# Kernel optimization log

Measured on AMD Instinct MI355X. Metric: run time of the kernel, lower is better.

Reference implementation:

```python
import jax, jax.numpy as jnp
import numpy as np

H, P, G, N, K, CS = 64, 64, 8, 128, 4, 256
HID = 2048
INTER = H * P                      # 4096
CONV_D = INTER + 2 * G * N         # 6144
PROJ = INTER + CONV_D + H          # 10304
EPS = 1e-5


def setup_inputs() -> dict:
    key = jax.random.key(0)
    ks = jax.random.split(key, 4)
    B_, L_ = 2, 2048
    return {
        "hidden_states": jax.random.normal(ks[0], (B_, L_, HID), jnp.float32),
        "in_proj_w": jax.random.normal(ks[1], (PROJ, HID), jnp.float32) * 0.02,
        "conv_w": jax.random.normal(ks[2], (CONV_D, K), jnp.float32) * 0.2,
        "conv_b": jnp.zeros((CONV_D,), jnp.float32),
        "dt_bias": jnp.ones((H,), jnp.float32),
        "A_log": jnp.log(jnp.arange(1, H + 1, dtype=jnp.float32)),
        "D": jnp.ones((H,), jnp.float32),
        "norm_w": jnp.ones((INTER,), jnp.float32),
        "out_proj_w": jax.random.normal(ks[3], (HID, INTER), jnp.float32) * 0.02,
    }


def reference(hidden_states, in_proj_w, conv_w, conv_b, dt_bias, A_log, D, norm_w, out_proj_w):
    b, l, _ = hidden_states.shape
    r = H // G  # heads per group

    zxbcdt = hidden_states @ in_proj_w.T                      # [b,l,PROJ]
    z = zxbcdt[..., :INTER]
    xBC = zxbcdt[..., INTER:INTER + CONV_D]
    dt = zxbcdt[..., INTER + CONV_D:]                          # [b,l,H]

    # causal depthwise conv1d (kernel K, left pad K-1) + SiLU
    xp = jnp.pad(xBC, ((0, 0), (K - 1, 0), (0, 0)))
    conv = conv_b
    for i in range(K):
        conv = conv + conv_w[:, i] * xp[:, i:i + l, :]
    xBC = jax.nn.silu(conv)

    x = xBC[..., :INTER]
    Bm = xBC[..., INTER:INTER + G * N]
    Cm = xBC[..., INTER + G * N:]

    dt = jax.nn.softplus(dt + dt_bias)                         # [b,l,H]
    A = -jnp.exp(A_log)                                        # [H]

    nc = l // CS
    x_c = x.reshape(b, nc, CS, G, r, P)
    dt_c = dt.reshape(b, nc, CS, G, r)
    B_c = Bm.reshape(b, nc, CS, G, N)
    C_c = Cm.reshape(b, nc, CS, G, N)

    dA = dt_c * A.reshape(G, r)                                # [b,nc,c,g,r]
    dA_cs = jnp.cumsum(dA, axis=2)                             # inclusive cumsum over chunk

    # intra-chunk: L[i,j] = exp(dA_cs[i]-dA_cs[j]) for i>=j
    diff = dA_cs[:, :, :, None] - dA_cs[:, :, None]            # [b,nc,i,j,g,r]
    mask = jnp.tril(jnp.ones((CS, CS), bool))[None, None, :, :, None, None]
    Lmat = jnp.exp(jnp.where(mask, diff, -jnp.inf))
    CB = jnp.einsum('bzign,bzjgn->bzijg', C_c, B_c)            # per-group C·B
    M = CB[..., None] * Lmat * dt_c[:, :, None]                # [b,nc,i,j,g,r]
    Y_diag = jnp.einsum('bzijgr,bzjgrp->bzigrp', M, x_c)

    # per-chunk end states
    w = jnp.exp(dA_cs[:, :, -1:] - dA_cs) * dt_c               # decay to chunk end * dt
    states = jnp.einsum('bzjgn,bzjgr,bzjgrp->bzgrpn', B_c, w, x_c)  # [b,nc,g,r,p,n]
    chunk_decay = jnp.exp(dA_cs[:, :, -1])                     # [b,nc,g,r]

    def step(S, inp):
        d, s = inp
        return d[..., None, None] * S + s, S                   # emit state BEFORE chunk

    init = jnp.zeros((b, G, r, P, N), x.dtype)
    _, prev = jax.lax.scan(step, init, (jnp.moveaxis(chunk_decay, 1, 0), jnp.moveaxis(states, 1, 0)))
    prev = jnp.moveaxis(prev, 0, 1)                            # [b,nc,g,r,p,n]

    Y_off = jnp.einsum('bzign,bzgrpn->bzigrp', C_c, prev) * jnp.exp(dA_cs)[..., None]

    Y = (Y_diag + Y_off).reshape(b, l, H, P) + D[:, None] * x.reshape(b, l, H, P)
    y = Y.reshape(b, l, INTER)

    # gated RMSNorm, norm_before_gate=True: out = rmsnorm(y) * silu(z)
    var = jnp.mean(y * y, axis=-1, keepdims=True)
    y = norm_w * (y * jax.lax.rsqrt(var + EPS)) * jax.nn.silu(z)

    return y @ out_proj_w.T
```

## Files before the change

kernel.cpp:

```cpp
#include <hip/hip_runtime.h>
#include <hip/hip_bf16.h>
#include <cstdint>
#include <cstddef>

#define H_     64
#define P_     64
#define G_     8
#define N_     128
#define K_     4
#define CS_    256
#define HID_   2048
#define INTER_ 4096
#define CONVD_ 6144
#define PROJ_  10304
#define ZSTR_  10240
#define B_     2
#define L_     2048
#define NC_    8
#define ML_    4096
#define EPS_   1e-5f

typedef unsigned short ushort_t;
typedef __attribute__((ext_vector_type(8))) short short8;
typedef __attribute__((ext_vector_type(4))) float f32x4;

__device__ inline float b2f(ushort_t v) {
  unsigned u = ((unsigned)v) << 16;
  float f;
  __builtin_memcpy(&f, &u, 4);
  return f;
}
__device__ inline ushort_t f2b(float f) {
  unsigned u;
  __builtin_memcpy(&u, &f, 4);
  u = u + 0x7FFFu + ((u >> 16) & 1u);
  return (ushort_t)(u >> 16);
}
__device__ inline void ld_bf8(const ushort_t* p, float* f) {
  uint4 u = *(const uint4*)p;
  const ushort_t* s = (const ushort_t*)&u;
#pragma unroll
  for (int c = 0; c < 8; ++c) f[c] = b2f(s[c]);
}
__device__ inline void st_bf8(ushort_t* p, const float* f) {
  uint4 u;
  ushort_t* s = (ushort_t*)&u;
#pragma unroll
  for (int c = 0; c < 8; ++c) s[c] = f2b(f[c]);
  *(uint4*)p = u;
}

__global__ __launch_bounds__(256) void cast1_k(const float* __restrict__ hs,
                                               const float* __restrict__ w_in,
                                               ushort_t* __restrict__ hsb,
                                               ushort_t* __restrict__ w_inb) {
  size_t e8 = ((size_t)blockIdx.x * 256 + threadIdx.x) * 8;
  const float* src;
  ushort_t* dst;
  const size_t HSN = (size_t)ML_ * HID_;
  if (e8 < HSN) { src = hs + e8; dst = hsb + e8; }
  else          { src = w_in + (e8 - HSN); dst = w_inb + (e8 - HSN); }
  float4 a = *(const float4*)src;
  float4 b = *(const float4*)(src + 4);
  float v[8] = {a.x, a.y, a.z, a.w, b.x, b.y, b.z, b.w};
  st_bf8(dst, v);
}

__global__ __launch_bounds__(256) void cast2_k(const float* __restrict__ w_out,
                                               ushort_t* __restrict__ w_outb) {
  size_t e8 = ((size_t)blockIdx.x * 256 + threadIdx.x) * 8;
  float4 a = *(const float4*)(w_out + e8);
  float4 b = *(const float4*)(w_out + e8 + 4);
  float v[8] = {a.x, a.y, a.z, a.w, b.x, b.y, b.z, b.w};
  st_bf8(w_outb + e8, v);
}

typedef const __attribute__((address_space(1))) unsigned int gu32;
typedef __attribute__((address_space(3))) unsigned int lu32;
__device__ __forceinline__ void gl_lds16(const ushort_t* g, ushort_t* l) {
  __builtin_amdgcn_global_load_lds((gu32*)g, (lu32*)l, 16, 0, 0);
}

template<int N> __device__ __forceinline__ void wait_vmcnt() {
  if constexpr (N == 8)      asm volatile("s_waitcnt vmcnt(8)" ::: "memory");
  else if constexpr (N == 6) asm volatile("s_waitcnt vmcnt(6)" ::: "memory");
  else if constexpr (N == 4) asm volatile("s_waitcnt vmcnt(4)" ::: "memory");
  else if constexpr (N == 3) asm volatile("s_waitcnt vmcnt(3)" ::: "memory");
  else                       asm volatile("s_waitcnt vmcnt(0)" ::: "memory");
}

template<int MR>
__device__ __forceinline__ void gemm_core(const ushort_t* __restrict__ Ag,
                                          const ushort_t* __restrict__ Bg,
                                          int lda, int ldb, int nkt,
                                          int bm, int bn, int brmax,
                                          ushort_t* __restrict__ As,
                                          ushort_t* __restrict__ Bs,
                                          f32x4 (&acc)[MR / 32][4]) {
  constexpr int MF = MR / 32;
  constexpr int ASLOT = MR * 32;
  constexpr int BSLOT = 256 * 32;
  constexpr int LPT = (MR == 256) ? 4 : 3;
  const int t = threadIdx.x;
  const int w = t >> 6, l = t & 63;
  const int wm = w >> 2, wn = w & 3;
  const int ml = l & 15, q = l >> 4;
  const int swz = (ml >> 1) & 3;
  const int aoff = (wm * (MR / 2) + ml) * 32 + ((q ^ swz) << 3);
  const int boff = (wn * 64 + ml) * 32 + ((q ^ swz) << 3);
  const int permc = (((l & 3) ^ ((l >> 3) & 3)) << 3);
  const ushort_t* ag0 = Ag + (size_t)(bm + (MR / 8) * w + (l >> 2)) * lda + permc;
  const ushort_t* ag1 = ag0 + (size_t)16 * lda;
  int br0 = bn + 32 * w + (l >> 2);      if (br0 > brmax) br0 = brmax;
  int br1 = bn + 32 * w + 16 + (l >> 2); if (br1 > brmax) br1 = brmax;
  const ushort_t* bg0 = Bg + (size_t)br0 * ldb + permc;
  const ushort_t* bg1 = Bg + (size_t)br1 * ldb + permc;
  ushort_t* alw = As + ((MR == 256) ? (2 * w * 512) : (w * 512));
  ushort_t* blw = Bs + 2 * w * 512;

#define STAGE_A_(kt_)                                                        \
  { const int k_ = (kt_) << 5;                                               \
    ushort_t* sa_ = alw + ((kt_) & 3) * ASLOT;                               \
    gl_lds16(ag0 + k_, sa_);                                                 \
    if (MR == 256) gl_lds16(ag1 + k_, sa_ + 512); }
#define STAGE_B_(kt_)                                                        \
  { const int k_ = (kt_) << 5;                                               \
    ushort_t* sb_ = blw + ((kt_) & 3) * BSLOT;                               \
    gl_lds16(bg0 + k_, sb_);                                                 \
    gl_lds16(bg1 + k_, sb_ + 512); }

  STAGE_A_(0); STAGE_B_(0);
  STAGE_A_(1); STAGE_B_(1);
  STAGE_A_(2); STAGE_B_(2);

#pragma unroll
  for (int i = 0; i < MF; ++i)
#pragma unroll
    for (int j = 0; j < 4; ++j) acc[i][j] = (f32x4){0.f, 0.f, 0.f, 0.f};

#pragma unroll 1
  for (int kt = 0; kt < nkt; ++kt) {
    const ushort_t* Asl = As + (kt & 3) * ASLOT;
    const ushort_t* Bsl = Bs + (kt & 3) * BSLOT;
    if (kt + 2 < nkt)      wait_vmcnt<2 * LPT>();
    else if (kt + 1 < nkt) wait_vmcnt<LPT>();
    else                   wait_vmcnt<0>();
    __builtin_amdgcn_s_barrier();
    asm volatile("" ::: "memory");
    const bool st = (kt + 3) < nkt;
    short8 bfr[4], af[MF / 2];
#pragma unroll
    for (int nf = 0; nf < 4; ++nf)
      bfr[nf] = *(const short8*)(Bsl + boff + nf * 512);
#pragma unroll
    for (int mf = 0; mf < MF / 2; ++mf)
      af[mf] = *(const short8*)(Asl + aoff + mf * 512);
    if (st) STAGE_A_(kt + 3);
    __builtin_amdgcn_s_setprio(1);
#pragma unroll
    for (int mf = 0; mf < MF / 2; ++mf)
#pragma unroll
      for (int nf = 0; nf < 4; ++nf)
        acc[mf][nf] = __builtin_amdgcn_mfma_f32_16x16x32_bf16(af[mf], bfr[nf], acc[mf][nf], 0, 0, 0);
    __builtin_amdgcn_s_setprio(0);
#pragma unroll
    for (int mf = 0; mf < MF / 2; ++mf)
      af[mf] = *(const short8*)(Asl + aoff + (mf + MF / 2) * 512);
    if (st) STAGE_B_(kt + 3);
    __builtin_amdgcn_s_setprio(1);
#pragma unroll
    for (int mf = 0; mf < MF / 2; ++mf)
#pragma unroll
      for (int nf = 0; nf < 4; ++nf)
        acc[mf + MF / 2][nf] = __builtin_amdgcn_mfma_f32_16x16x32_bf16(af[mf], bfr[nf], acc[mf + MF / 2][nf], 0, 0, 0);
    __builtin_amdgcn_s_setprio(0);
  }
#undef STAGE_A_
#undef STAGE_B_
}

__global__ __launch_bounds__(512, 2) void gemm1_256(const ushort_t* __restrict__ hsb,
                                                    const ushort_t* __restrict__ w_inb,
                                                    ushort_t* __restrict__ zb,
                                                    float* __restrict__ dtraw) {
  __shared__ __align__(16) ushort_t As[4 * 8192];
  __shared__ __align__(16) ushort_t Bs[4 * 8192];
  int bid = blockIdx.x;
  int wg = (bid & 7) * 82 + (bid >> 3);
  int tm = wg & 15, tn = wg >> 4;
  int bm = tm * 256, bn = tn * 256;
  f32x4 acc[8][4];
  gemm_core<256>(hsb, w_inb, HID_, HID_, HID_ / 32, bm, bn, PROJ_ - 1, As, Bs, acc);
  int t = threadIdx.x, w = t >> 6, l = t & 63;
  int wm = w >> 2, wn = w & 3, ml = l & 15, quad = l >> 4;
  int rb = bm + wm * 128 + quad * 4;
  int cb = bn + wn * 64 + ml;
  if (tn < 40) {
#pragma unroll
    for (int mf = 0; mf < 8; ++mf)
#pragma unroll
      for (int r = 0; r < 4; ++r) {
        size_t row = (size_t)(rb + mf * 16 + r) * ZSTR_;
#pragma unroll
        for (int nf = 0; nf < 4; ++nf)
          zb[row + cb + nf * 16] = f2b(acc[mf][nf][r]);
      }
  } else if (wn == 0) {
#pragma unroll
    for (int mf = 0; mf < 8; ++mf)
#pragma unroll
      for (int r = 0; r < 4; ++r) {
        size_t row = (size_t)(rb + mf * 16 + r) * 64;
#pragma unroll
        for (int nf = 0; nf < 4; ++nf)
          dtraw[row + ml + nf * 16] = acc[mf][nf][r];
      }
  }
}

__global__ __launch_bounds__(512, 2) void gemm2_128(const ushort_t* __restrict__ Ab,
                                                    const ushort_t* __restrict__ Bb,
                                                    float* __restrict__ C) {
  __shared__ __align__(16) ushort_t As[4 * 4096];
  __shared__ __align__(16) ushort_t Bs[4 * 8192];
  int bid = blockIdx.x;
  int wg = (bid & 7) * 32 + (bid >> 3);
  int tm = wg & 31, tn = wg >> 5;
  int bm = tm * 128, bn = tn * 256;
  f32x4 acc[4][4];
  gemm_core<128>(Ab, Bb, CONVD_, INTER_, INTER_ / 32, bm, bn, HID_ - 1, As, Bs, acc);
  int t = threadIdx.x, w = t >> 6, l = t & 63;
  int wm = w >> 2, wn = w & 3, ml = l & 15, quad = l >> 4;
  int rb = bm + wm * 64 + quad * 4;
  int cb = bn + wn * 64 + ml;
#pragma unroll
  for (int mf = 0; mf < 4; ++mf)
#pragma unroll
    for (int r = 0; r < 4; ++r) {
      size_t row = (size_t)(rb + mf * 16 + r) * HID_;
#pragma unroll
      for (int nf = 0; nf < 4; ++nf)
        C[row + cb + nf * 16] = acc[mf][nf][r];
    }
}

#define CROWS_ 8
__global__ __launch_bounds__(256) void conv_silu_k(const ushort_t* __restrict__ zb,
                                                   const float* __restrict__ cw,
                                                   const float* __restrict__ cb,
                                                   ushort_t* __restrict__ xcb) {
  int grp = blockIdx.x & 511;
  int seg = blockIdx.x >> 9;
  int u = threadIdx.x;
  int c8 = seg * 2048 + u * 8;
  int row0 = grp * CROWS_;
  int l0 = row0 & (L_ - 1);

  float wv[K_][8], bias[8];
  {
    const float4* wp = (const float4*)(cw + (size_t)c8 * K_);
#pragma unroll
    for (int c = 0; c < 8; ++c) {
      float4 w4 = wp[c];
      wv[0][c] = w4.x; wv[1][c] = w4.y; wv[2][c] = w4.z; wv[3][c] = w4.w;
    }
    float4 b0 = *(const float4*)(cb + c8);
    float4 b1 = *(const float4*)(cb + c8 + 4);
    bias[0] = b0.x; bias[1] = b0.y; bias[2] = b0.z; bias[3] = b0.w;
    bias[4] = b1.x; bias[5] = b1.y; bias[6] = b1.z; bias[7] = b1.w;
  }

  const ushort_t* xin = zb + (size_t)row0 * ZSTR_ + INTER_ + c8;
  ushort_t* xout = xcb + (size_t)row0 * CONVD_ + c8;

  float win[4][8];
#pragma unroll
  for (int i = 0; i < 3; ++i) {
    if (l0 > 0) {
      ld_bf8(xin + (ptrdiff_t)(i - 3) * ZSTR_, win[i]);
    } else {
#pragma unroll
      for (int c = 0; c < 8; ++c) win[i][c] = 0.f;
    }
  }
#pragma unroll
  for (int r = 0; r < CROWS_; ++r) {
    ld_bf8(xin + (size_t)r * ZSTR_, win[(r + 3) & 3]);
    float a[8];
#pragma unroll
    for (int c = 0; c < 8; ++c) {
      float v = bias[c];
      v = fmaf(wv[0][c], win[(r + 0) & 3][c], v);
      v = fmaf(wv[1][c], win[(r + 1) & 3][c], v);
      v = fmaf(wv[2][c], win[(r + 2) & 3][c], v);
      v = fmaf(wv[3][c], win[(r + 3) & 3][c], v);
      a[c] = v / (1.f + __expf(-v));
    }
    st_bf8(xout + (size_t)r * CONVD_, a);
  }
}

__global__ __launch_bounds__(256) void dt_scan_k(const float* __restrict__ dtraw,
                                                 const float* __restrict__ dt_bias,
                                                 const float* __restrict__ A_log,
                                                 float* __restrict__ dtp,
                                                 float* __restrict__ dacs,
                                                 float* __restrict__ cdec) {
  int bzh = blockIdx.x;
  int h = bzh & 63, z = (bzh >> 6) & 7, b = bzh >> 9;
  int i = threadIdx.x;
  size_t row = (size_t)b * L_ + z * CS_ + i;
  float dv = dtraw[row * 64 + h] + dt_bias[h];
  float sp = (dv > 20.f) ? dv : log1pf(expf(dv));
  float v = sp * (-expf(A_log[h]));
  __shared__ float sm[256];
  sm[i] = v;
  __syncthreads();
  for (int off = 1; off < 256; off <<= 1) {
    float add = (i >= off) ? sm[i - off] : 0.f;
    __syncthreads();
    sm[i] += add;
    __syncthreads();
  }
  float cs = sm[i];
  size_t ob = ((size_t)b * H_ + h) * L_ + z * CS_ + i;
  dtp[ob] = sp;
  dacs[ob] = cs;
  if (i == CS_ - 1) cdec[bzh] = expf(cs);
}

__global__ __launch_bounds__(256) void cb_k(const ushort_t* __restrict__ xcb,
                                            ushort_t* __restrict__ CBo) {
  int jt = blockIdx.x & 3, it = blockIdx.x >> 2;
  if (jt > it) return;
  int bzg = blockIdx.y;
  int g = bzg & 7, z = (bzg >> 3) & 7, b = bzg >> 6;
  int t = threadIdx.x;
  int tx = t & 15, ty = t >> 4;
  __shared__ float CtT[64][68];
  __shared__ float BtT[64][68];
  size_t rowbase = (size_t)b * L_ + (size_t)z * CS_;
  float acc[4][4];
#pragma unroll
  for (int i = 0; i < 4; ++i)
#pragma unroll
    for (int j = 0; j < 4; ++j) acc[i][j] = 0.f;

  for (int half = 0; half < 2; ++half) {
    int nb = half * 64;
    __syncthreads();
#pragma unroll
    for (int u = 0; u < 2; ++u) {
      int idx = t + u * 256;
      int rr = idx >> 3, f = idx & 7;
      float cv[8], bv[8];
      ld_bf8(xcb + (rowbase + it * 64 + rr) * CONVD_ + INTER_ + G_ * N_ + g * N_ + nb + f * 8, cv);
      ld_bf8(xcb + (rowbase + jt * 64 + rr) * CONVD_ + INTER_ + g * N_ + nb + f * 8, bv);
#pragma unroll
      for (int c = 0; c < 8; ++c) { CtT[f * 8 + c][rr] = cv[c]; BtT[f * 8 + c][rr] = bv[c]; }
    }
    __syncthreads();
    for (int n = 0; n < 64; ++n) {
      float4 cv = *(const float4*)&CtT[n][ty * 4];
      float4 bv = *(const float4*)&BtT[n][tx * 4];
      float cc[4] = {cv.x, cv.y, cv.z, cv.w};
      float bb[4] = {bv.x, bv.y, bv.z, bv.w};
#pragma unroll
      for (int i = 0; i < 4; ++i)
#pragma unroll
        for (int j = 0; j < 4; ++j) acc[i][j] = fmaf(cc[i], bb[j], acc[i][j]);
    }
  }
  size_t cbase = ((size_t)((b * 8 + z) * 8 + g)) * (CS_ * CS_);
#pragma unroll
  for (int i = 0; i < 4; ++i) {
    int row = it * 64 + ty * 4 + i;
    ushort4 v;
    v.x = f2b(acc[i][0]); v.y = f2b(acc[i][1]); v.z = f2b(acc[i][2]); v.w = f2b(acc[i][3]);
    *(ushort4*)(CBo + cbase + (size_t)row * CS_ + jt * 64 + tx * 4) = v;
  }
}

__global__ __launch_bounds__(256) void states_mfma(const ushort_t* __restrict__ xcb,
                                                   const float* __restrict__ dacs,
                                                   const float* __restrict__ dtp,
                                                   float* __restrict__ st) {
  int bzh = blockIdx.x;
  int h = bzh & 63, z = (bzh >> 6) & 7, b = bzh >> 9;
  int g = h >> 3;
  int t = threadIdx.x;
  int wv = t >> 6, lane = t & 63;
  int ml = lane & 15, ko = (lane >> 4) * 8;
  __shared__ float ws[256];
  __shared__ __align__(16) ushort_t Xw[64 * 136];
  __shared__ __align__(16) ushort_t Bt[128 * 136];
  size_t base = ((size_t)b * H_ + h) * L_ + z * CS_;
  float dlast = dacs[base + CS_ - 1];
  ws[t] = __expf(dlast - dacs[base + t]) * dtp[base + t];
  size_t rowbase = (size_t)b * L_ + z * CS_;
  f32x4 acc[4][2];
#pragma unroll
  for (int i = 0; i < 4; ++i) {
    acc[i][0] = (f32x4){0.f, 0.f, 0.f, 0.f};
    acc[i][1] = (f32x4){0.f, 0.f, 0.f, 0.f};
  }
  for (int half = 0; half < 2; ++half) {
    int j0 = half * 128;
    __syncthreads();
    {
      int jl = t >> 1, pseg = (t & 1) * 32;
      const ushort_t* xr = xcb + (rowbase + j0 + jl) * CONVD_ + h * P_ + pseg;
      float wj = ws[j0 + jl];
#pragma unroll
      for (int q = 0; q < 4; ++q) {
        float v[8];
        ld_bf8(xr + q * 8, v);
#pragma unroll
        for (int c = 0; c < 8; ++c) Xw[(pseg + q * 8 + c) * 136 + jl] = f2b(v[c] * wj);
      }
    }
    {
      int jl = t >> 1, nseg = (t & 1) * 64;
      const ushort_t* br = xcb + (rowbase + j0 + jl) * CONVD_ + INTER_ + g * N_ + nseg;
#pragma unroll
      for (int q = 0; q < 8; ++q) {
        uint4 raw = *(const uint4*)(br + q * 8);
        const ushort_t* s = (const ushort_t*)&raw;
#pragma unroll
        for (int c = 0; c < 8; ++c) Bt[(nseg + q * 8 + c) * 136 + jl] = s[c];
      }
    }
    __syncthreads();
#pragma unroll
    for (int k0 = 0; k0 < 128; k0 += 32) {
      short8 af[4], bf2[2];
#pragma unroll
      for (int mf = 0; mf < 4; ++mf)
        af[mf] = *(const short8*)(Xw + (mf * 16 + ml) * 136 + k0 + ko);
#pragma unroll
      for (int nf = 0; nf < 2; ++nf)
        bf2[nf] = *(const short8*)(Bt + (wv * 32 + nf * 16 + ml) * 136 + k0 + ko);
#pragma unroll
      for (int mf = 0; mf < 4; ++mf)
#pragma unroll
        for (int nf = 0; nf < 2; ++nf)
          acc[mf][nf] = __builtin_amdgcn_mfma_f32_16x16x32_bf16(af[mf], bf2[nf], acc[mf][nf], 0, 0, 0);
    }
  }
  float* outp = st + ((size_t)((b * 8 + z) * H_ + h)) * (P_ * N_);
  int quad = lane >> 4;
#pragma unroll
  for (int mf = 0; mf < 4; ++mf)
#pragma unroll
    for (int nf = 0; nf < 2; ++nf) {
      int n = wv * 32 + nf * 16 + ml;
#pragma unroll
      for (int r = 0; r < 4; ++r) {
        int p = mf * 16 + quad * 4 + r;
        outp[(size_t)p * N_ + n] = acc[mf][nf][r];
      }
    }
}

__global__ __launch_bounds__(256) void scan_k(float* __restrict__ st,
                                              const float* __restrict__ cdec) {
  size_t idx = (size_t)blockIdx.x * 256 + threadIdx.x;
  int b = (int)(idx >> 19);
  size_t rem = idx & 524287;
  int h = (int)(rem >> 13);
  float S = 0.f;
#pragma unroll
  for (int z = 0; z < NC_; ++z) {
    size_t off = (size_t)(b * 8 + z) * 524288 + rem;
    float old = st[off];
    st[off] = S;
    S = cdec[(b * 8 + z) * H_ + h] * S + old;
  }
}

__global__ __launch_bounds__(256) void y_mfma(const ushort_t* xcb,
                                              const ushort_t* __restrict__ CB,
                                              const float* __restrict__ pv,
                                              const float* __restrict__ dacs,
                                              const float* __restrict__ dtp,
                                              const float* __restrict__ Dw,
                                              ushort_t* Yx) {
  int bzh = blockIdx.x;
  int h = bzh & 63, z = (bzh >> 6) & 7, b = bzh >> 9;
  int g = h >> 3;
  int t = threadIdx.x;
  int wv = t >> 6, lane = t & 63;
  int ml = lane & 15, quad = lane >> 4, ko = quad * 8;
  __shared__ __align__(16) ushort_t Ms[256 * 40];
  __shared__ __align__(16) ushort_t XsYs[18432];
  __shared__ __align__(16) ushort_t Ps[64 * 136];
  __shared__ float dAs[256], dts[256];

  size_t rowbase = (size_t)b * L_ + z * CS_;
  {
    size_t base = ((size_t)b * H_ + h) * L_ + z * CS_;
    dAs[t] = dacs[base + t];
    dts[t] = dtp[base + t];
  }
  {
    int p = t >> 2, c0 = (t & 3) * 32;
    const float* pr = pv + ((size_t)((b * 8 + z) * H_ + h)) * (P_ * N_) + (size_t)p * N_ + c0;
    ushort_t* dst = Ps + p * 136 + c0;
#pragma unroll
    for (int u = 0; u < 4; ++u) {
      float4 a = *(const float4*)(pr + u * 8);
      float4 bq = *(const float4*)(pr + u * 8 + 4);
      float v[8] = {a.x, a.y, a.z, a.w, bq.x, bq.y, bq.z, bq.w};
      st_bf8(dst + u * 8, v);
    }
  }
  {
    const ushort_t* xr = xcb + (rowbase + t) * CONVD_ + h * P_;
    ushort_t* Xs = XsYs;
#pragma unroll
    for (int q = 0; q < 8; ++q) {
      uint4 raw = *(const uint4*)(xr + q * 8);
      const ushort_t* s = (const ushort_t*)&raw;
#pragma unroll
      for (int c = 0; c < 8; ++c) Xs[(q * 8 + c) * 264 + t] = s[c];
    }
  }

  f32x4 acc[4][4];
#pragma unroll
  for (int i = 0; i < 4; ++i)
#pragma unroll
    for (int j = 0; j < 4; ++j) acc[i][j] = (f32x4){0.f, 0.f, 0.f, 0.f};

  int cOff = INTER_ + G_ * N_ + g * N_;
#pragma unroll
  for (int k0 = 0; k0 < 128; k0 += 32) {
    __syncthreads();
#pragma unroll
    for (int u = 0; u < 4; ++u) {
      int sid = u * 256 + t;
      int row = sid >> 2, kc = (sid & 3) * 8;
      gl_lds16(xcb + (rowbase + row) * CONVD_ + cOff + k0 + kc,
               Ms + (size_t)(u * 256 + wv * 64) * 8);
    }
    __syncthreads();
    short8 af[4], bf[4];
#pragma unroll
    for (int mf = 0; mf < 4; ++mf)
      af[mf] = *(const short8*)(Ps + (mf * 16 + ml) * 136 + k0 + ko);
#pragma unroll
    for (int nf = 0; nf < 4; ++nf)
      bf[nf] = *(const short8*)(Ms + (wv * 64 + nf * 16 + ml) * 32 + ko);
#pragma unroll
    for (int mf = 0; mf < 4; ++mf)
#pragma unroll
      for (int nf = 0; nf < 4; ++nf)
        acc[mf][nf] = __builtin_amdgcn_mfma_f32_16x16x32_bf16(af[mf], bf[nf], acc[mf][nf], 0, 0, 0);
  }
#pragma unroll
  for (int nf = 0; nf < 4; ++nf) {
    float e = __expf(dAs[wv * 64 + nf * 16 + ml]);
#pragma unroll
    for (int mf = 0; mf < 4; ++mf) {
      acc[mf][nf][0] *= e; acc[mf][nf][1] *= e;
      acc[mf][nf][2] *= e; acc[mf][nf][3] *= e;
    }
  }

  float dAi_t = dAs[t];
  size_t cbase = ((size_t)((b * 8 + z) * 8 + g)) * (CS_ * CS_) + (size_t)t * CS_;
  const ushort_t* Xs = XsYs;
  for (int j0 = 0; j0 < 256; j0 += 32) {
    __syncthreads();
    {
      const ushort_t* cbr = CB + cbase + j0;
      ushort_t* mrow = Ms + t * 40;
#pragma unroll
      for (int q = 0; q < 4; ++q) {
        float cv[8], o[8];
        ld_bf8(cbr + q * 8, cv);
#pragma unroll
        for (int c = 0; c < 8; ++c) {
          int j = j0 + q * 8 + c;
          float m = cv[c] * __expf(dAi_t - dAs[j]) * dts[j];
          o[c] = (j <= t) ? m : 0.f;
        }
        st_bf8(mrow + q * 8, o);
      }
    }
    __syncthreads();
    short8 af[4], bf[4];
#pragma unroll
    for (int mf = 0; mf < 4; ++mf)
      af[mf] = *(const short8*)(Xs + (mf * 16 + ml) * 264 + j0 + ko);
#pragma unroll
    for (int nf = 0; nf < 4; ++nf)
      bf[nf] = *(const short8*)(Ms + (wv * 64 + nf * 16 + ml) * 40 + ko);
#pragma unroll
    for (int mf = 0; mf < 4; ++mf)
#pragma unroll
      for (int nf = 0; nf < 4; ++nf)
        acc[mf][nf] = __builtin_amdgcn_mfma_f32_16x16x32_bf16(af[mf], bf[nf], acc[mf][nf], 0, 0, 0);
  }

  __syncthreads();
  ushort_t* Ys = XsYs;
#pragma unroll
  for (int mf = 0; mf < 4; ++mf)
#pragma unroll
    for (int nf = 0; nf < 4; ++nf) {
      int iw = wv * 64 + nf * 16 + ml;
      int pb = mf * 16 + quad * 4;
      uint2 pk;
      ushort_t* s = (ushort_t*)&pk;
      s[0] = f2b(acc[mf][nf][0]); s[1] = f2b(acc[mf][nf][1]);
      s[2] = f2b(acc[mf][nf][2]); s[3] = f2b(acc[mf][nf][3]);
      *(uint2*)(Ys + iw * 72 + pb) = pk;
    }
  __syncthreads();
  {
    float Dh = Dw[h];
    const ushort_t* xr = xcb + (rowbase + t) * CONVD_ + h * P_;
    ushort_t* yr = Yx + (rowbase + t) * CONVD_ + h * P_;
#pragma unroll
    for (int q = 0; q < 8; ++q) {
      float xv[8], yv[8], o[8];
      ld_bf8(xr + q * 8, xv);
      ld_bf8(Ys + t * 72 + q * 8, yv);
#pragma unroll
      for (int c = 0; c < 8; ++c) o[c] = yv[c] + Dh * xv[c];
      st_bf8(yr + q * 8, o);
    }
  }
}

__global__ __launch_bounds__(256) void rms_gate_k(ushort_t* __restrict__ Y,
                                                  const ushort_t* __restrict__ zb,
                                                  const float* __restrict__ nw) {
  int row = blockIdx.x;
  int t = threadIdx.x;
  ushort_t* y = Y + (size_t)row * CONVD_;
  const ushort_t* zp = zb + (size_t)row * ZSTR_;
  float v[2][8];
  float s = 0.f;
#pragma unroll
  for (int u = 0; u < 2; ++u) {
    ld_bf8(y + u * 2048 + t * 8, v[u]);
#pragma unroll
    for (int c = 0; c < 8; ++c) s += v[u][c] * v[u][c];
  }
#pragma unroll
  for (int off = 32; off > 0; off >>= 1) s += __shfl_down(s, off);
  __shared__ float red[4];
  if ((t & 63) == 0) red[t >> 6] = s;
  __syncthreads();
  float tot = red[0] + red[1] + red[2] + red[3];
  float rstd = rsqrtf(tot * (1.f / INTER_) + EPS_);
#pragma unroll
  for (int u = 0; u < 2; ++u) {
    int c0 = u * 2048 + t * 8;
    float zv[8], o[8];
    ld_bf8(zp + c0, zv);
    float4 w0 = *(const float4*)(nw + c0);
    float4 w1 = *(const float4*)(nw + c0 + 4);
    float wv[8] = {w0.x, w0.y, w0.z, w0.w, w1.x, w1.y, w1.z, w1.w};
#pragma unroll
    for (int c = 0; c < 8; ++c)
      o[c] = wv[c] * v[u][c] * rstd * (zv[c] / (1.f + __expf(-zv[c])));
    st_bf8(y + c0, o);
  }
}

extern "C" void kernel_launch(void* const* d_in, const int* in_sizes, int n_in,
                              void* d_out, int out_size, void* d_ws, size_t ws_size,
                              hipStream_t stream) {
  const float* hs    = (const float*)d_in[0];
  const float* w_in  = (const float*)d_in[1];
  const float* cw    = (const float*)d_in[2];
  const float* cb    = (const float*)d_in[3];
  const float* dtb   = (const float*)d_in[4];
  const float* alog  = (const float*)d_in[5];
  const float* Dw    = (const float*)d_in[6];
  const float* nw    = (const float*)d_in[7];
  const float* w_out = (const float*)d_in[8];
  float* out = (float*)d_out;

  char* base = (char*)d_ws;
  ushort_t* zb    = (ushort_t*)(base);
  ushort_t* xcb   = (ushort_t*)(base + 83886080);
  float*    dtraw = (float*)(base + 134217728);
  float*    dtp   = (float*)(base + 135266304);
  float*    dacs  = (float*)(base + 136314880);
  float*    cdec  = (float*)(base + 137363456);
  char*     R1    = base + 137367552;
  char*     R2    = base + 154144768;
  ushort_t* hsb    = (ushort_t*)R1;
  ushort_t* cbuf   = (ushort_t*)R1;
  ushort_t* w_outb = (ushort_t*)R1;
  ushort_t* w_inb  = (ushort_t*)R2;
  float*    st     = (float*)R2;

  cast1_k<<<14400, 256, 0, stream>>>(hs, w_in, hsb, w_inb);
  gemm1_256<<<656, 512, 0, stream>>>(hsb, w_inb, zb, dtraw);
  conv_silu_k<<<1536, 256, 0, stream>>>(zb, cw, cb, xcb);
  dt_scan_k<<<B_ * NC_ * H_, 256, 0, stream>>>(dtraw, dtb, alog, dtp, dacs, cdec);
  cb_k<<<dim3(16, B_ * NC_ * G_), 256, 0, stream>>>(xcb, cbuf);
  states_mfma<<<B_ * NC_ * H_, 256, 0, stream>>>(xcb, dacs, dtp, st);
  scan_k<<<(B_ * H_ * P_ * N_) / 256, 256, 0, stream>>>(st, cdec);
  y_mfma<<<B_ * NC_ * H_, 256, 0, stream>>>(xcb, cbuf, st, dacs, dtp, Dw, xcb);
  rms_gate_k<<<ML_, 256, 0, stream>>>(xcb, zb, nw);
  cast2_k<<<4096, 256, 0, stream>>>(w_out, w_outb);
  gemm2_128<<<256, 512, 0, stream>>>(xcb, w_outb, out);
}
```

Baseline: 649.5 us.

## Merge small kernels, transpose dt layout, add intra-iteration GEMM barriers

Merges conv_silu and dt_scan into one launch and rms_gate and the out-proj weight cast into another, so two kernel launches and their tail gaps go away. The dt output of the first GEMM is stored head-major so the scan kernel reads consecutive tokens with coalesced loads. It also adds extra workgroup barriers between the LDS read/stage phases and the MFMA phases inside the GEMM main loop, which may help keep waves in step but adds synchronisation cost.

```diff
diff --git a/kernel.cpp b/kernel.cpp
--- a/kernel.cpp
+++ b/kernel.cpp
@@ -66,15 +66,6 @@
   st_bf8(dst, v);
 }
 
-__global__ __launch_bounds__(256) void cast2_k(const float* __restrict__ w_out,
-                                               ushort_t* __restrict__ w_outb) {
-  size_t e8 = ((size_t)blockIdx.x * 256 + threadIdx.x) * 8;
-  float4 a = *(const float4*)(w_out + e8);
-  float4 b = *(const float4*)(w_out + e8 + 4);
-  float v[8] = {a.x, a.y, a.z, a.w, b.x, b.y, b.z, b.w};
-  st_bf8(w_outb + e8, v);
-}
-
 typedef const __attribute__((address_space(1))) unsigned int gu32;
 typedef __attribute__((address_space(3))) unsigned int lu32;
 __device__ __forceinline__ void gl_lds16(const ushort_t* g, ushort_t* l) {
@@ -87,6 +78,10 @@
   else if constexpr (N == 4) asm volatile("s_waitcnt vmcnt(4)" ::: "memory");
   else if constexpr (N == 3) asm volatile("s_waitcnt vmcnt(3)" ::: "memory");
   else                       asm volatile("s_waitcnt vmcnt(0)" ::: "memory");
+}
+__device__ __forceinline__ void phase_barrier() {
+  __builtin_amdgcn_s_barrier();
+  asm volatile("" ::: "memory");
 }
 
 template<int MR>
@@ -145,8 +140,7 @@
     if (kt + 2 < nkt)      wait_vmcnt<2 * LPT>();
     else if (kt + 1 < nkt) wait_vmcnt<LPT>();
     else                   wait_vmcnt<0>();
-    __builtin_amdgcn_s_barrier();
-    asm volatile("" ::: "memory");
+    phase_barrier();
     const bool st = (kt + 3) < nkt;
     short8 bfr[4], af[MF / 2];
 #pragma unroll
@@ -156,6 +150,7 @@
     for (int mf = 0; mf < MF / 2; ++mf)
       af[mf] = *(const short8*)(Asl + aoff + mf * 512);
     if (st) STAGE_A_(kt + 3);
+    phase_barrier();
     __builtin_amdgcn_s_setprio(1);
 #pragma unroll
     for (int mf = 0; mf < MF / 2; ++mf)
@@ -163,10 +158,12 @@
       for (int nf = 0; nf < 4; ++nf)
         acc[mf][nf] = __builtin_amdgcn_mfma_f32_16x16x32_bf16(af[mf], bfr[nf], acc[mf][nf], 0, 0, 0);
     __builtin_amdgcn_s_setprio(0);
+    phase_barrier();
 #pragma unroll
     for (int mf = 0; mf < MF / 2; ++mf)
       af[mf] = *(const short8*)(Asl + aoff + (mf + MF / 2) * 512);
     if (st) STAGE_B_(kt + 3);
+    phase_barrier();
     __builtin_amdgcn_s_setprio(1);
 #pragma unroll
     for (int mf = 0; mf < MF / 2; ++mf)
@@ -210,10 +207,10 @@
     for (int mf = 0; mf < 8; ++mf)
 #pragma unroll
       for (int r = 0; r < 4; ++r) {
-        size_t row = (size_t)(rb + mf * 16 + r) * 64;
+        int tok = rb + mf * 16 + r;
 #pragma unroll
         for (int nf = 0; nf < 4; ++nf)
-          dtraw[row + ml + nf * 16] = acc[mf][nf][r];
+          dtraw[(size_t)(ml + nf * 16) * ML_ + tok] = acc[mf][nf][r];
       }
   }
 }
@@ -245,88 +242,89 @@
 }
 
 #define CROWS_ 8
-__global__ __launch_bounds__(256) void conv_silu_k(const ushort_t* __restrict__ zb,
-                                                   const float* __restrict__ cw,
-                                                   const float* __restrict__ cb,
-                                                   ushort_t* __restrict__ xcb) {
-  int grp = blockIdx.x & 511;
-  int seg = blockIdx.x >> 9;
-  int u = threadIdx.x;
-  int c8 = seg * 2048 + u * 8;
-  int row0 = grp * CROWS_;
-  int l0 = row0 & (L_ - 1);
-
-  float wv[K_][8], bias[8];
-  {
-    const float4* wp = (const float4*)(cw + (size_t)c8 * K_);
-#pragma unroll
-    for (int c = 0; c < 8; ++c) {
-      float4 w4 = wp[c];
-      wv[0][c] = w4.x; wv[1][c] = w4.y; wv[2][c] = w4.z; wv[3][c] = w4.w;
-    }
-    float4 b0 = *(const float4*)(cb + c8);
-    float4 b1 = *(const float4*)(cb + c8 + 4);
-    bias[0] = b0.x; bias[1] = b0.y; bias[2] = b0.z; bias[3] = b0.w;
-    bias[4] = b1.x; bias[5] = b1.y; bias[6] = b1.z; bias[7] = b1.w;
-  }
-
-  const ushort_t* xin = zb + (size_t)row0 * ZSTR_ + INTER_ + c8;
-  ushort_t* xout = xcb + (size_t)row0 * CONVD_ + c8;
-
-  float win[4][8];
-#pragma unroll
-  for (int i = 0; i < 3; ++i) {
-    if (l0 > 0) {
-      ld_bf8(xin + (ptrdiff_t)(i - 3) * ZSTR_, win[i]);
-    } else {
-#pragma unroll
-      for (int c = 0; c < 8; ++c) win[i][c] = 0.f;
-    }
-  }
-#pragma unroll
-  for (int r = 0; r < CROWS_; ++r) {
-    ld_bf8(xin + (size_t)r * ZSTR_, win[(r + 3) & 3]);
-    float a[8];
-#pragma unroll
-    for (int c = 0; c < 8; ++c) {
-      float v = bias[c];
-      v = fmaf(wv[0][c], win[(r + 0) & 3][c], v);
-      v = fmaf(wv[1][c], win[(r + 1) & 3][c], v);
-      v = fmaf(wv[2][c], win[(r + 2) & 3][c], v);
-      v = fmaf(wv[3][c], win[(r + 3) & 3][c], v);
-      a[c] = v / (1.f + __expf(-v));
-    }
-    st_bf8(xout + (size_t)r * CONVD_, a);
-  }
-}
-
-__global__ __launch_bounds__(256) void dt_scan_k(const float* __restrict__ dtraw,
+__global__ __launch_bounds__(256) void conv_dt_k(const ushort_t* __restrict__ zb,
+                                                 const float* __restrict__ cw,
+                                                 const float* __restrict__ cb,
+                                                 ushort_t* __restrict__ xcb,
+                                                 const float* __restrict__ dtraw,
                                                  const float* __restrict__ dt_bias,
                                                  const float* __restrict__ A_log,
                                                  float* __restrict__ dtp,
                                                  float* __restrict__ dacs,
                                                  float* __restrict__ cdec) {
-  int bzh = blockIdx.x;
-  int h = bzh & 63, z = (bzh >> 6) & 7, b = bzh >> 9;
-  int i = threadIdx.x;
-  size_t row = (size_t)b * L_ + z * CS_ + i;
-  float dv = dtraw[row * 64 + h] + dt_bias[h];
-  float sp = (dv > 20.f) ? dv : log1pf(expf(dv));
-  float v = sp * (-expf(A_log[h]));
   __shared__ float sm[256];
-  sm[i] = v;
-  __syncthreads();
-  for (int off = 1; off < 256; off <<= 1) {
-    float add = (i >= off) ? sm[i - off] : 0.f;
-    __syncthreads();
-    sm[i] += add;
-    __syncthreads();
-  }
-  float cs = sm[i];
-  size_t ob = ((size_t)b * H_ + h) * L_ + z * CS_ + i;
-  dtp[ob] = sp;
-  dacs[ob] = cs;
-  if (i == CS_ - 1) cdec[bzh] = expf(cs);
+  int bid = blockIdx.x;
+  if (bid < 1536) {
+    int grp = bid & 511;
+    int seg = bid >> 9;
+    int u = threadIdx.x;
+    int c8 = seg * 2048 + u * 8;
+    int row0 = grp * CROWS_;
+    int l0 = row0 & (L_ - 1);
+
+    float wv[K_][8], bias[8];
+    {
+      const float4* wp = (const float4*)(cw + (size_t)c8 * K_);
+#pragma unroll
+      for (int c = 0; c < 8; ++c) {
+        float4 w4 = wp[c];
+        wv[0][c] = w4.x; wv[1][c] = w4.y; wv[2][c] = w4.z; wv[3][c] = w4.w;
+      }
+      float4 b0 = *(const float4*)(cb + c8);
+      float4 b1 = *(const float4*)(cb + c8 + 4);
+      bias[0] = b0.x; bias[1] = b0.y; bias[2] = b0.z; bias[3] = b0.w;
+      bias[4] = b1.x; bias[5] = b1.y; bias[6] = b1.z; bias[7] = b1.w;
+    }
+    const ushort_t* xin = zb + (size_t)row0 * ZSTR_ + INTER_ + c8;
+    ushort_t* xout = xcb + (size_t)row0 * CONVD_ + c8;
+
+    float win[4][8];
+#pragma unroll
+    for (int i = 0; i < 3; ++i) {
+      if (l0 > 0) {
+        ld_bf8(xin + (ptrdiff_t)(i - 3) * ZSTR_, win[i]);
+      } else {
+#pragma unroll
+        for (int c = 0; c < 8; ++c) win[i][c] = 0.f;
+      }
+    }
+#pragma unroll
+    for (int r = 0; r < CROWS_; ++r) {
+      ld_bf8(xin + (size_t)r * ZSTR_, win[(r + 3) & 3]);
+      float a[8];
+#pragma unroll
+      for (int c = 0; c < 8; ++c) {
+        float v = bias[c];
+        v = fmaf(wv[0][c], win[(r + 0) & 3][c], v);
+        v = fmaf(wv[1][c], win[(r + 1) & 3][c], v);
+        v = fmaf(wv[2][c], win[(r + 2) & 3][c], v);
+        v = fmaf(wv[3][c], win[(r + 3) & 3][c], v);
+        a[c] = v / (1.f + __expf(-v));
+      }
+      st_bf8(xout + (size_t)r * CONVD_, a);
+    }
+  } else {
+    int bzh = bid - 1536;
+    int h = bzh & 63, z = (bzh >> 6) & 7, b = bzh >> 9;
+    int i = threadIdx.x;
+    size_t row = (size_t)b * L_ + z * CS_ + i;
+    float dv = dtraw[(size_t)h * ML_ + row] + dt_bias[h];
+    float sp = (dv > 20.f) ? dv : log1pf(expf(dv));
+    float v = sp * (-expf(A_log[h]));
+    sm[i] = v;
+    __syncthreads();
+    for (int off = 1; off < 256; off <<= 1) {
+      float add = (i >= off) ? sm[i - off] : 0.f;
+      __syncthreads();
+      sm[i] += add;
+      __syncthreads();
+    }
+    float cs = sm[i];
+    size_t ob = ((size_t)b * H_ + h) * L_ + z * CS_ + i;
+    dtp[ob] = sp;
+    dacs[ob] = cs;
+    if (i == CS_ - 1) cdec[bzh] = expf(cs);
+  }
 }
 
 __global__ __launch_bounds__(256) void cb_k(const ushort_t* __restrict__ xcb,
@@ -634,11 +632,23 @@
   }
 }
 
-__global__ __launch_bounds__(256) void rms_gate_k(ushort_t* __restrict__ Y,
-                                                  const ushort_t* __restrict__ zb,
-                                                  const float* __restrict__ nw) {
-  int row = blockIdx.x;
+__global__ __launch_bounds__(256) void rms_cast2_k(ushort_t* __restrict__ Y,
+                                                   const ushort_t* __restrict__ zb,
+                                                   const float* __restrict__ nw,
+                                                   const float* __restrict__ w_out,
+                                                   ushort_t* __restrict__ w_outb) {
+  __shared__ float red[4];
+  int bid = blockIdx.x;
   int t = threadIdx.x;
+  if (bid >= ML_) {
+    size_t e8 = ((size_t)(bid - ML_) * 256 + t) * 8;
+    float4 a = *(const float4*)(w_out + e8);
+    float4 b = *(const float4*)(w_out + e8 + 4);
+    float v[8] = {a.x, a.y, a.z, a.w, b.x, b.y, b.z, b.w};
+    st_bf8(w_outb + e8, v);
+    return;
+  }
+  int row = bid;
   ushort_t* y = Y + (size_t)row * CONVD_;
   const ushort_t* zp = zb + (size_t)row * ZSTR_;
   float v[2][8];
@@ -651,7 +661,6 @@
   }
 #pragma unroll
   for (int off = 32; off > 0; off >>= 1) s += __shfl_down(s, off);
-  __shared__ float red[4];
   if ((t & 63) == 0) red[t >> 6] = s;
   __syncthreads();
   float tot = red[0] + red[1] + red[2] + red[3];
@@ -702,13 +711,11 @@
 
   cast1_k<<<14400, 256, 0, stream>>>(hs, w_in, hsb, w_inb);
   gemm1_256<<<656, 512, 0, stream>>>(hsb, w_inb, zb, dtraw);
-  conv_silu_k<<<1536, 256, 0, stream>>>(zb, cw, cb, xcb);
-  dt_scan_k<<<B_ * NC_ * H_, 256, 0, stream>>>(dtraw, dtb, alog, dtp, dacs, cdec);
+  conv_dt_k<<<2560, 256, 0, stream>>>(zb, cw, cb, xcb, dtraw, dtb, alog, dtp, dacs, cdec);
   cb_k<<<dim3(16, B_ * NC_ * G_), 256, 0, stream>>>(xcb, cbuf);
   states_mfma<<<B_ * NC_ * H_, 256, 0, stream>>>(xcb, dacs, dtp, st);
   scan_k<<<(B_ * H_ * P_ * N_) / 256, 256, 0, stream>>>(st, cdec);
   y_mfma<<<B_ * NC_ * H_, 256, 0, stream>>>(xcb, cbuf, st, dacs, dtp, Dw, xcb);
-  rms_gate_k<<<ML_, 256, 0, stream>>>(xcb, zb, nw);
-  cast2_k<<<4096, 256, 0, stream>>>(w_out, w_outb);
+  rms_cast2_k<<<8192, 256, 0, stream>>>(xcb, zb, nw, w_out, w_outb);
   gemm2_128<<<256, 512, 0, stream>>>(xcb, w_outb, out);
 }
```

Measured after the change: 669.3 us. 3.1% more time.
